# Kernel optimization log

Hardware: AMD Instinct MI355X
Metric: run time of the kernel (lower is better)

## Reference

```python
import jax, jax.numpy as jnp
import numpy as np

NUM_HEADS = 8
DIM = 256
NUM_Q = 1


def setup_inputs() -> dict:
    key = jax.random.key(0)
    ks = jax.random.split(key, 10)
    B, H, W, C = 4, 56, 56, DIM
    mask_h = mask_w = 7
    WinNum = mask_h * mask_w
    x = jax.random.normal(ks[0], (B, H, W, C), dtype=jnp.float32)
    clstoken = jax.random.normal(ks[1], (B, NUM_Q, C), dtype=jnp.float32)
    mask = jax.random.bernoulli(ks[2], 0.3, (B, WinNum, WinNum))
    # ensure each window attends to itself (avoid fully-masked rows)
    eye = jnp.eye(WinNum, dtype=bool)[None]
    mask = jnp.logical_or(mask, eye)
    Wqkv = jax.random.normal(ks[3], (C, 3 * C), dtype=jnp.float32) * (C ** -0.5)
    bqkv = jnp.zeros((3 * C,), dtype=jnp.float32)
    Wo = jax.random.normal(ks[4], (C, C), dtype=jnp.float32) * (C ** -0.5)
    bo = jnp.zeros((C,), dtype=jnp.float32)
    lepe_k = jax.random.normal(ks[5], (3, 3, 1, C), dtype=jnp.float32) * 0.1  # depthwise HWIO
    lepe_b = jnp.zeros((C,), dtype=jnp.float32)
    return {"x": x, "clstoken": clstoken, "mask": mask, "mask_h": mask_h,
            "mask_w": mask_w, "Wqkv": Wqkv, "bqkv": bqkv, "Wo": Wo, "bo": bo,
            "lepe_k": lepe_k, "lepe_b": lepe_b}


def _forward(x, clstoken, mask, mask_h, mask_w, Wqkv, bqkv, Wo, bo, lepe_k, lepe_b):
    B, H, W, C = x.shape
    num_q = clstoken.shape[1]
    Nh = NUM_HEADS
    Hd = C // Nh
    Win_h, Win_w = H // mask_h, W // mask_w
    WinPix = Win_h * Win_w
    WinNum = mask_h * mask_w
    L_win = H * W
    scale = C ** -0.5

    qkv = x @ Wqkv + bqkv                       # [B,H,W,3C]
    q, k, v = jnp.split(qkv, 3, axis=-1)
    qkv_cls = clstoken @ Wqkv + bqkv            # [B,Q,3C]
    q_cls, k_cls, v_cls = jnp.split(qkv_cls, 3, axis=-1)

    # depthwise lepe conv on v (NHWC)
    lepe = jax.lax.conv_general_dilated(
        v, lepe_k, window_strides=(1, 1), padding='SAME',
        dimension_numbers=('NHWC', 'HWIO', 'NHWC'), feature_group_count=C) + lepe_b

    def to_win(t):  # b (j h)(i w)(Nh Hd) -> b Nh (j i h w) Hd
        t = t.reshape(B, mask_h, Win_h, mask_w, Win_w, Nh, Hd)
        t = t.transpose(0, 5, 1, 3, 2, 4, 6)
        return t.reshape(B, Nh, L_win, Hd)

    def cls_heads(t):  # b q (Nh Hd) -> b Nh q Hd
        return t.reshape(B, num_q, Nh, Hd).transpose(0, 2, 1, 3)

    q_all = jnp.concatenate([to_win(q), cls_heads(q_cls)], axis=2)
    k_all = jnp.concatenate([to_win(k), cls_heads(k_cls)], axis=2)
    v_all = jnp.concatenate([to_win(v), cls_heads(v_cls)], axis=2)

    # token-level block mask; cls block (id WinNum) is globally visible
    blk = jnp.concatenate([jnp.arange(L_win) // WinPix,
                           jnp.full((num_q,), WinNum)])
    mask_ext = jnp.pad(mask, ((0, 0), (0, 1), (0, 1)), constant_values=True)
    tok_mask = mask_ext[:, blk[:, None], blk[None, :]]  # [B,L,L]

    scores = jnp.einsum('bnqd,bnkd->bnqk', q_all, k_all) * scale
    neg = jnp.finfo(scores.dtype).min
    scores = jnp.where(tok_mask[:, None], scores, neg)
    attn = jax.nn.softmax(scores, axis=-1)
    out = jnp.einsum('bnqk,bnkd->bnqd', attn, v_all)   # [B,Nh,L,Hd]

    cls_out = out[:, :, -num_q:, :]
    x_out = out[:, :, :-num_q, :]
    # b Nh (j i h w) Hd -> b (j h)(i w)(Nh Hd)
    x_out = x_out.reshape(B, Nh, mask_h, mask_w, Win_h, Win_w, Hd)
    x_out = x_out.transpose(0, 2, 4, 3, 5, 1, 6).reshape(B, H, W, C)
    cls_out = cls_out.transpose(0, 2, 1, 3).reshape(B, num_q, C)

    x_out = (x_out + lepe) @ Wo + bo
    cls_out = cls_out @ Wo + bo
    return x_out, cls_out


def reference(x, clstoken, mask, mask_h, mask_w, Wqkv, bqkv, Wo, bo, lepe_k, lepe_b):
    return _forward(x, clstoken, mask, mask_h, mask_w, Wqkv, bqkv, Wo, bo, lepe_k, lepe_b)
```

## Files before the change

kernel.cpp:

```cpp
#include <hip/hip_runtime.h>
#include <math.h>

#define B_      4
#define NH      8
#define HD      32
#define WINNUM  49
#define LWIN    3136
#define NTOK    3137
#define NPIX    12544
#define MROWS   12548
#define SCALE_L2E 0.09016844005556021f

typedef _Float16 half_t;
using half8  = __attribute__((ext_vector_type(8))) half_t;
using half4  = __attribute__((ext_vector_type(4))) half_t;
using f32x4  = __attribute__((ext_vector_type(4))) float;
using f32x16 = __attribute__((ext_vector_type(16))) float;

__device__ __forceinline__ unsigned pack2(float a, float b) {
    auto h = __builtin_amdgcn_cvt_pkrtz(a, b);
    return __builtin_bit_cast(unsigned, h);
}
__device__ __forceinline__ half8 as_h8(int4 v) {
    return __builtin_bit_cast(half8, v);
}

__global__ __launch_bounds__(256)
void prep(const float* __restrict__ x, const float* __restrict__ cls,
          const float* __restrict__ Wqkv, const float* __restrict__ Wo,
          half_t* __restrict__ xh, half_t* __restrict__ Wqkvt, half_t* __restrict__ Wot)
{
    const int idx = blockIdx.x * 256 + threadIdx.x;
    const int stride = gridDim.x * 256;
    for (int i = idx; i < MROWS * 256; i += stride) {
        int row = i >> 8, c = i & 255;
        float v = (row < NPIX) ? x[i] : cls[(row - NPIX) * 256 + c];
        xh[i] = (half_t)v;
    }
    for (int i = idx; i < 768 * 256; i += stride) {
        int n = i >> 8, k = i & 255;
        Wqkvt[i] = (half_t)Wqkv[k * 768 + n];
    }
    for (int i = idx; i < 256 * 256; i += stride) {
        int n = i >> 8, k = i & 255;
        Wot[i] = (half_t)Wo[k * 256 + n];
    }
}

__global__ __launch_bounds__(256)
void qkv_gemm(const half_t* __restrict__ xh, const half_t* __restrict__ Bt,
              const float* __restrict__ bqkv,
              half_t* __restrict__ qh, half_t* __restrict__ kh,
              half_t* __restrict__ khcls, half_t* __restrict__ vh,
              half_t* __restrict__ vplain)
{
    __shared__ __align__(16) short As[2][128 * 40];
    __shared__ __align__(16) short Bs[2][128 * 40];
    const int m0 = blockIdx.y * 128, n0 = blockIdx.x * 128;
    const int tid = threadIdx.x;
    const int lane = tid & 63, wv = tid >> 6;
    const int wm = wv >> 1, wn = wv & 1;
    const int qi = lane & 15, g = lane >> 4;
    f32x4 acc[4][4] = {};

    int4 ra[2], rb[2];
    auto issue = [&](int k0) {
#pragma unroll
        for (int i = 0; i < 2; ++i) {
            int ch = tid + 256 * i;
            int row = ch >> 2, kc = (ch & 3) * 8;
            int m = m0 + row;
            ra[i] = (m < MROWS) ? *(const int4*)(xh + (size_t)m * 256 + k0 + kc)
                                : make_int4(0, 0, 0, 0);
            rb[i] = *(const int4*)(Bt + (size_t)(n0 + row) * 256 + k0 + kc);
        }
    };
    auto commit = [&](int bu) {
#pragma unroll
        for (int i = 0; i < 2; ++i) {
            int ch = tid + 256 * i;
            int row = ch >> 2, kc = (ch & 3) * 8;
            *(int4*)&As[bu][row * 40 + kc] = ra[i];
            *(int4*)&Bs[bu][row * 40 + kc] = rb[i];
        }
    };

    issue(0); commit(0);
    __syncthreads();
    int buf = 0;
    for (int s = 0; s < 8; ++s) {
        if (s < 7) issue((s + 1) * 32);
        half8 af[4], bf[4];
#pragma unroll
        for (int f = 0; f < 4; ++f) {
            af[f] = *(const half8*)&As[buf][(wm * 64 + f * 16 + qi) * 40 + g * 8];
            bf[f] = *(const half8*)&Bs[buf][(wn * 64 + f * 16 + qi) * 40 + g * 8];
        }
#pragma unroll
        for (int fm = 0; fm < 4; ++fm)
#pragma unroll
            for (int fn = 0; fn < 4; ++fn)
                acc[fm][fn] = __builtin_amdgcn_mfma_f32_16x16x32_f16(af[fm], bf[fn], acc[fm][fn], 0, 0, 0);
        if (s < 7) commit(buf ^ 1);
        __syncthreads();
        buf ^= 1;
    }

    const int part = n0 >> 8;
    int nhv[4], dv[4];
    float bq[4];
#pragma unroll
    for (int fn = 0; fn < 4; ++fn) {
        int n = n0 + wn * 64 + fn * 16 + qi;
        bq[fn] = bqkv[n];
        int c = n & 255;
        nhv[fn] = c >> 5; dv[fn] = c & 31;
    }
#pragma unroll
    for (int fm = 0; fm < 4; ++fm) {
#pragma unroll
        for (int r = 0; r < 4; ++r) {
            int m = m0 + wm * 64 + fm * 16 + g * 4 + r;
            if (m >= MROWS) continue;
            int b, tok;
            if (m < NPIX) {
                b = m / LWIN;
                int p = m - b * LWIN;
                int hh = p / 56, ww = p - hh * 56;
                tok = ((hh >> 3) * 7 + (ww >> 3)) * 64 + ((hh & 7) << 3) + (ww & 7);
            } else { b = m - NPIX; tok = LWIN; }
#pragma unroll
            for (int fn = 0; fn < 4; ++fn) {
                float val = acc[fm][fn][r] + bq[fn];
                size_t bh = (size_t)(b * NH + nhv[fn]);
                int d = dv[fn];
                if (part == 0) {
                    qh[(bh * NTOK + tok) * 32 + d] = (half_t)(val * SCALE_L2E);
                } else if (part == 1) {
                    if (tok < LWIN) kh[(bh * WINNUM + (tok >> 6)) * 2560 + (tok & 63) * 40 + d] = (half_t)val;
                    else            khcls[bh * 32 + d] = (half_t)val;
                } else {
                    vplain[(bh * NTOK + tok) * 32 + d] = (half_t)val;
                    if (tok < LWIN) vh[(bh * WINNUM + (tok >> 6)) * 2560 + d * 80 + (tok & 63)] = (half_t)val;
                }
            }
        }
    }
}

__global__ __launch_bounds__(128)
void win_attn(const half_t* __restrict__ qh, const half_t* __restrict__ kh,
              const half_t* __restrict__ khcls, const half_t* __restrict__ vh,
              const half_t* __restrict__ vplain, const int* __restrict__ mask,
              half_t* __restrict__ tg, float* __restrict__ clspart)
{
    const int id = blockIdx.x;
    const int tid = threadIdx.x;
    __shared__ __align__(16) short Plds[2][32 * 72];
    __shared__ float redc[2 * 33];
    const int lane = tid & 63, wv = tid >> 6;

    if (id >= 1568) {
        const int cid = id - 1568;
        const int bh = cid >> 3;
        const int chunk = cid & 7;
        const int wstart = chunk * 6;
        const int nw = (chunk < 7) ? 6 : 7;
        const int nkeys = nw * 64;

        float q[32];
        {
            const half_t* qp = qh + ((size_t)bh * NTOK + LWIN) * 32;
#pragma unroll
            for (int d = 0; d < 32; ++d) q[d] = (float)qp[d];
        }
        float l = 0.f, o[32];
#pragma unroll
        for (int d = 0; d < 32; ++d) o[d] = 0.f;

        const half_t* kwb = kh + (size_t)bh * (WINNUM * 2560) + wstart * 2560;
        const half_t* vb  = vplain + ((size_t)bh * NTOK + wstart * 64) * 32;

        for (int kk = tid; kk < nkeys; kk += 128) {
            const half_t* kp = kwb + (kk >> 6) * 2560 + (kk & 63) * 40;
            float s = 0.f;
#pragma unroll
            for (int c8 = 0; c8 < 4; ++c8) {
                half8 kv = *(const half8*)(kp + c8 * 8);
#pragma unroll
                for (int j = 0; j < 8; ++j) s += q[c8 * 8 + j] * (float)kv[j];
            }
            float pp = exp2f(s);
            l += pp;
            const half_t* vp = vb + (size_t)kk * 32;
#pragma unroll
            for (int c8 = 0; c8 < 4; ++c8) {
                half8 vvv = *(const half8*)(vp + c8 * 8);
#pragma unroll
                for (int j = 0; j < 8; ++j) o[c8 * 8 + j] += pp * (float)vvv[j];
            }
        }
        if (chunk == 7 && tid == 0) {
            const half_t* kp = khcls + bh * 32;
            float s = 0.f;
#pragma unroll
            for (int d = 0; d < 32; ++d) s += q[d] * (float)kp[d];
            float pp = exp2f(s);
            l += pp;
            const half_t* vp = vplain + ((size_t)bh * NTOK + LWIN) * 32;
#pragma unroll
            for (int d = 0; d < 32; ++d) o[d] += pp * (float)vp[d];
        }
#pragma unroll
        for (int off = 1; off < 64; off <<= 1) {
            l += __shfl_xor(l, off);
#pragma unroll
            for (int d = 0; d < 32; ++d) o[d] += __shfl_xor(o[d], off);
        }
        if (lane == 0) {
#pragma unroll
            for (int d = 0; d < 32; ++d) redc[wv * 33 + d] = o[d];
            redc[wv * 33 + 32] = l;
        }
        __syncthreads();
        if (tid < 33) {
            clspart[(bh * 8 + chunk) * 33 + tid] = redc[tid] + redc[33 + tid];
        }
        return;
    }

    const int sw = (id & 7) * 196 + (id >> 3);
    const int wi = sw % 49;
    const int bh = sw / 49;
    const int b = bh >> 3, nh = bh & 7;

    const int qc = lane & 31;
    const int hb = lane >> 5;
    const int qbase = wi * 64 + wv * 32;

    const half_t* qp = qh + ((size_t)bh * NTOK + qbase + qc) * 32 + hb * 8;
    half8 aq0 = as_h8(*(const int4*)(qp));
    half8 aq1 = as_h8(*(const int4*)(qp + 16));

    half8 onesA = {};
    if (qc == 0) {
#pragma unroll
        for (int j = 0; j < 8; ++j) onesA[j] = (half_t)1.0f;
    }

    const f32x16 Z16 = {0.f,0.f,0.f,0.f,0.f,0.f,0.f,0.f,0.f,0.f,0.f,0.f,0.f,0.f,0.f,0.f};
    f32x16 acc   = Z16;
    f32x16 acc_l = Z16;

    const int* mrow = mask + (b * WINNUM + wi) * WINNUM;
    int mv = (lane < WINNUM) ? mrow[lane] : 0;
    unsigned long long rem = __ballot(mv != 0);

    const half_t* kwin = kh + (size_t)bh * (WINNUM * 2560);
    const half_t* vwin = vh + (size_t)bh * (WINNUM * 2560);

    short* pw = &Plds[wv][qc * 72];
    const short* prd = &Plds[wv][qc * 72 + hb * 8];

    while (rem) {
        const int wj = __builtin_ctzll(rem);
        rem &= rem - 1;
        const half_t* kb = kwin + wj * 2560 + qc * 40 + hb * 8;
        const half_t* vb = vwin + wj * 2560 + qc * 80 + hb * 8;
        int4 kf00 = *(const int4*)(kb);
        int4 kf01 = *(const int4*)(kb + 16);
        int4 kf10 = *(const int4*)(kb + 1280);
        int4 kf11 = *(const int4*)(kb + 1296);
        int4 vf0 = *(const int4*)(vb);
        int4 vf1 = *(const int4*)(vb + 16);
        int4 vf2 = *(const int4*)(vb + 32);
        int4 vf3 = *(const int4*)(vb + 48);

        f32x16 st[2];
        __builtin_amdgcn_s_setprio(1);
        st[0] = __builtin_amdgcn_mfma_f32_32x32x16_f16(as_h8(kf00), aq0, Z16, 0, 0, 0);
        st[1] = __builtin_amdgcn_mfma_f32_32x32x16_f16(as_h8(kf10), aq0, Z16, 0, 0, 0);
        st[0] = __builtin_amdgcn_mfma_f32_32x32x16_f16(as_h8(kf01), aq1, st[0], 0, 0, 0);
        st[1] = __builtin_amdgcn_mfma_f32_32x32x16_f16(as_h8(kf11), aq1, st[1], 0, 0, 0);
        __builtin_amdgcn_s_setprio(0);

#pragma unroll
        for (int t = 0; t < 2; ++t)
#pragma unroll
            for (int rb = 0; rb < 4; ++rb) {
                float p0 = exp2f(st[t][4 * rb + 0]);
                float p1 = exp2f(st[t][4 * rb + 1]);
                float p2 = exp2f(st[t][4 * rb + 2]);
                float p3 = exp2f(st[t][4 * rb + 3]);
                *(uint2*)&pw[t * 32 + 8 * rb + 4 * hb] =
                    make_uint2(pack2(p0, p1), pack2(p2, p3));
            }

        half8 pB0 = *(const half8*)(prd);
        half8 pB1 = *(const half8*)(prd + 16);
        half8 pB2 = *(const half8*)(prd + 32);
        half8 pB3 = *(const half8*)(prd + 48);
        __builtin_amdgcn_s_setprio(1);
        acc   = __builtin_amdgcn_mfma_f32_32x32x16_f16(as_h8(vf0), pB0, acc, 0, 0, 0);
        acc_l = __builtin_amdgcn_mfma_f32_32x32x16_f16(onesA, pB0, acc_l, 0, 0, 0);
        acc   = __builtin_amdgcn_mfma_f32_32x32x16_f16(as_h8(vf1), pB1, acc, 0, 0, 0);
        acc_l = __builtin_amdgcn_mfma_f32_32x32x16_f16(onesA, pB1, acc_l, 0, 0, 0);
        acc   = __builtin_amdgcn_mfma_f32_32x32x16_f16(as_h8(vf2), pB2, acc, 0, 0, 0);
        acc_l = __builtin_amdgcn_mfma_f32_32x32x16_f16(onesA, pB2, acc_l, 0, 0, 0);
        acc   = __builtin_amdgcn_mfma_f32_32x32x16_f16(as_h8(vf3), pB3, acc, 0, 0, 0);
        acc_l = __builtin_amdgcn_mfma_f32_32x32x16_f16(onesA, pB3, acc_l, 0, 0, 0);
        __builtin_amdgcn_s_setprio(0);
    }

    float lwin = __shfl(acc_l[0], qc);

    float sc = 0.f;
    {
        const half_t* kcb = khcls + bh * 32 + hb * 8;
        half8 kc0 = *(const half8*)(kcb);
        half8 kc1 = *(const half8*)(kcb + 16);
#pragma unroll
        for (int j = 0; j < 8; ++j)
            sc += (float)aq0[j] * (float)kc0[j] + (float)aq1[j] * (float)kc1[j];
        sc += __shfl_xor(sc, 32);
    }
    float pc = exp2f(sc);
    float l = lwin + pc;
    {
        const half_t* vcb = vplain + ((size_t)bh * NTOK + LWIN) * 32;
#pragma unroll
        for (int rb = 0; rb < 4; ++rb) {
            half4 vc = *(const half4*)(vcb + 8 * rb + 4 * hb);
#pragma unroll
            for (int r = 0; r < 4; ++r) acc[4 * rb + r] += pc * (float)vc[r];
        }
    }

    {
        float inv = 1.f / l;
        int kk = wv * 32 + qc;
        int hh = (wi / 7) * 8 + (kk >> 3);
        int ww = (wi % 7) * 8 + (kk & 7);
        size_t pix = (size_t)b * LWIN + hh * 56 + ww;
        half_t* tp = tg + pix * 256 + nh * 32;
#pragma unroll
        for (int rb = 0; rb < 4; ++rb) {
            half4 hv;
#pragma unroll
            for (int r = 0; r < 4; ++r) hv[r] = (half_t)(acc[4 * rb + r] * inv);
            *(half4*)(tp + 8 * rb + 4 * hb) = hv;
        }
    }
}

__global__ __launch_bounds__(256)
void lepe_add(const half_t* __restrict__ vplain, const float* __restrict__ lk,
              const float* __restrict__ lb, const float* __restrict__ clspart,
              half_t* __restrict__ tg)
{
    if (blockIdx.x == 1568) {
        const int c = threadIdx.x;
        const int nh = c >> 5, d = c & 31;
#pragma unroll
        for (int b = 0; b < 4; ++b) {
            int bh = b * NH + nh;
            float os = 0.f, ls = 0.f;
#pragma unroll
            for (int ch = 0; ch < 8; ++ch) {
                os += clspart[(bh * 8 + ch) * 33 + d];
                ls += clspart[(bh * 8 + ch) * 33 + 32];
            }
            tg[(size_t)(NPIX + b) * 256 + c] = (half_t)(os / ls);
        }
        return;
    }
    const int gidx = blockIdx.x * 256 + threadIdx.x;
    const int pix = gidx >> 5, cg = gidx & 31;
    const int c0 = cg * 8;
    const int b = pix / LWIN, p = pix - b * LWIN;
    const int hh = p / 56, ww = p - hh * 56;
    const int nh = c0 >> 5, d0 = c0 & 31;
    const half_t* vb = vplain + (size_t)(b * NH + nh) * NTOK * 32 + d0;

    float s[8];
#pragma unroll
    for (int j = 0; j < 8; ++j) s[j] = lb[c0 + j];
#pragma unroll
    for (int dh = -1; dh <= 1; ++dh) {
        int hn = hh + dh;
        if (hn < 0 || hn >= 56) continue;
#pragma unroll
        for (int dw = -1; dw <= 1; ++dw) {
            int wn = ww + dw;
            if (wn < 0 || wn >= 56) continue;
            int tok = ((hn >> 3) * 7 + (wn >> 3)) * 64 + ((hn & 7) << 3) + (wn & 7);
            half8 vvv = *(const half8*)(vb + (size_t)tok * 32);
            const float* kk = lk + ((dh + 1) * 3 + (dw + 1)) * 256 + c0;
#pragma unroll
            for (int j = 0; j < 8; ++j) s[j] += (float)vvv[j] * kk[j];
        }
    }
    half_t* tp = tg + (size_t)pix * 256 + c0;
    half8 cur = *(const half8*)tp;
    half8 outv;
#pragma unroll
    for (int j = 0; j < 8; ++j) outv[j] = (half_t)((float)cur[j] + s[j]);
    *(half8*)tp = outv;
}

__global__ __launch_bounds__(256)
void out_gemm(const half_t* __restrict__ th, const half_t* __restrict__ Bt,
              const float* __restrict__ bo, float* __restrict__ out)
{
    __shared__ __align__(16) short As[2][64 * 40];
    __shared__ __align__(16) short Bs[2][128 * 40];
    const int m0 = blockIdx.y * 64, n0 = blockIdx.x * 128;
    const int tid = threadIdx.x;
    const int lane = tid & 63, wv = tid >> 6;
    const int wm = wv >> 1, wn = wv & 1;
    const int qi = lane & 15, g = lane >> 4;
    f32x4 acc[2][4] = {};

    int4 ra, rb[2];
    auto issue = [&](int k0) {
        {
            int row = tid >> 2, kc = (tid & 3) * 8;
            int m = m0 + row;
            ra = (m < MROWS) ? *(const int4*)(th + (size_t)m * 256 + k0 + kc)
                             : make_int4(0, 0, 0, 0);
        }
#pragma unroll
        for (int i = 0; i < 2; ++i) {
            int ch = tid + 256 * i;
            int row = ch >> 2, kc = (ch & 3) * 8;
            rb[i] = *(const int4*)(Bt + (size_t)(n0 + row) * 256 + k0 + kc);
        }
    };
    auto commit = [&](int bu) {
        {
            int row = tid >> 2, kc = (tid & 3) * 8;
            *(int4*)&As[bu][row * 40 + kc] = ra;
        }
#pragma unroll
        for (int i = 0; i < 2; ++i) {
            int ch = tid + 256 * i;
            int row = ch >> 2, kc = (ch & 3) * 8;
            *(int4*)&Bs[bu][row * 40 + kc] = rb[i];
        }
    };

    issue(0); commit(0);
    __syncthreads();
    int buf = 0;
    for (int s = 0; s < 8; ++s) {
        if (s < 7) issue((s + 1) * 32);
        half8 af[2], bf[4];
#pragma unroll
        for (int f = 0; f < 2; ++f)
            af[f] = *(const half8*)&As[buf][(wm * 32 + f * 16 + qi) * 40 + g * 8];
#pragma unroll
        for (int f = 0; f < 4; ++f)
            bf[f] = *(const half8*)&Bs[buf][(wn * 64 + f * 16 + qi) * 40 + g * 8];
#pragma unroll
        for (int fm = 0; fm < 2; ++fm)
#pragma unroll
            for (int fn = 0; fn < 4; ++fn)
                acc[fm][fn] = __builtin_amdgcn_mfma_f32_16x16x32_f16(af[fm], bf[fn], acc[fm][fn], 0, 0, 0);
        if (s < 7) commit(buf ^ 1);
        __syncthreads();
        buf ^= 1;
    }

    float bov[4];
    int nn[4];
#pragma unroll
    for (int fn = 0; fn < 4; ++fn) {
        nn[fn] = n0 + wn * 64 + fn * 16 + qi;
        bov[fn] = bo[nn[fn]];
    }
#pragma unroll
    for (int fm = 0; fm < 2; ++fm)
#pragma unroll
        for (int r = 0; r < 4; ++r) {
            int m = m0 + wm * 32 + fm * 16 + g * 4 + r;
            if (m >= MROWS) continue;
#pragma unroll
            for (int fn = 0; fn < 4; ++fn)
                out[(size_t)m * 256 + nn[fn]] = acc[fm][fn][r] + bov[fn];
        }
}

extern "C" void kernel_launch(void* const* d_in, const int* in_sizes, int n_in,
                              void* d_out, int out_size, void* d_ws, size_t ws_size,
                              hipStream_t stream)
{
    const float* x    = (const float*)d_in[0];
    const float* cls  = (const float*)d_in[1];
    const int*   mask = (const int*)d_in[2];
    const float* Wqkv = (const float*)d_in[5];
    const float* bqkv = (const float*)d_in[6];
    const float* Wo   = (const float*)d_in[7];
    const float* bo   = (const float*)d_in[8];
    const float* lk   = (const float*)d_in[9];
    const float* lb   = (const float*)d_in[10];
    float* out = (float*)d_out;

    char* w = (char*)d_ws;
    half_t* xh     = (half_t*)w;  w += 6424576;
    half_t* qh     = (half_t*)w;  w += 6424576;
    half_t* kh     = (half_t*)w;  w += 8028160;
    half_t* khcls  = (half_t*)w;  w += 2048;
    half_t* vh     = (half_t*)w;  w += 8028160;
    half_t* vplain = (half_t*)w;  w += 6424576;
    half_t* Wqkvt  = (half_t*)w;  w += 393216;
    half_t* Wot    = (half_t*)w;  w += 131072;
    half_t* th     = (half_t*)w;  w += 6424576;
    float*  clspart= (float*)w;   w += 33792;

    prep<<<1600, 256, 0, stream>>>(x, cls, Wqkv, Wo, xh, Wqkvt, Wot);
    qkv_gemm<<<dim3(6, 99), 256, 0, stream>>>(xh, Wqkvt, bqkv, qh, kh, khcls, vh, vplain);
    win_attn<<<1824, 128, 0, stream>>>(qh, kh, khcls, vh, vplain, mask, th, clspart);
    lepe_add<<<1569, 256, 0, stream>>>(vplain, lk, lb, clspart, th);
    out_gemm<<<dim3(2, 197), 256, 0, stream>>>(th, Wot, bo, out);
}
```

Measured before the change: 125.2 us.

## Split window-attention key windows across wave pairs with double-buffered loads

Blocks for window attention grow from 128 to 256 threads. Each pair of waves now processes alternating visible key windows for the same 32 queries, and the two partial accumulators are combined through shared memory before normalization and the cls-token contribution. The main loop also double-buffers the K/V register loads so the next window's fetch is issued while the current one is computed. This aims to hide global-load latency and add parallelism per query tile, at the cost of more registers, an extra LDS reduction with two barriers, and a serial mask-splitting loop.

```diff
diff --git a/kernel.cpp b/kernel.cpp
--- a/kernel.cpp
+++ b/kernel.cpp
@@ -148,7 +148,7 @@
     }
 }
 
-__global__ __launch_bounds__(128)
+__global__ __launch_bounds__(256)
 void win_attn(const half_t* __restrict__ qh, const half_t* __restrict__ kh,
               const half_t* __restrict__ khcls, const half_t* __restrict__ vh,
               const half_t* __restrict__ vplain, const int* __restrict__ mask,
@@ -156,8 +156,8 @@
 {
     const int id = blockIdx.x;
     const int tid = threadIdx.x;
-    __shared__ __align__(16) short Plds[2][32 * 72];
-    __shared__ float redc[2 * 33];
+    __shared__ __align__(16) short Plds[4][32 * 72];
+    __shared__ float redc[4 * 33];
     const int lane = tid & 63, wv = tid >> 6;
 
     if (id >= 1568) {
@@ -181,7 +181,7 @@
         const half_t* kwb = kh + (size_t)bh * (WINNUM * 2560) + wstart * 2560;
         const half_t* vb  = vplain + ((size_t)bh * NTOK + wstart * 64) * 32;
 
-        for (int kk = tid; kk < nkeys; kk += 128) {
+        for (int kk = tid; kk < nkeys; kk += 256) {
             const half_t* kp = kwb + (kk >> 6) * 2560 + (kk & 63) * 40;
             float s = 0.f;
 #pragma unroll
@@ -224,7 +224,8 @@
         }
         __syncthreads();
         if (tid < 33) {
-            clspart[(bh * 8 + chunk) * 33 + tid] = redc[tid] + redc[33 + tid];
+            clspart[(bh * 8 + chunk) * 33 + tid] =
+                redc[tid] + redc[33 + tid] + redc[66 + tid] + redc[99 + tid];
         }
         return;
     }
@@ -234,9 +235,11 @@
     const int bh = sw / 49;
     const int b = bh >> 3, nh = bh & 7;
 
+    const int qhalf = wv & 1;
+    const int par   = wv >> 1;
     const int qc = lane & 31;
     const int hb = lane >> 5;
-    const int qbase = wi * 64 + wv * 32;
+    const int qbase = wi * 64 + qhalf * 32;
 
     const half_t* qp = qh + ((size_t)bh * NTOK + qbase + qc) * 32 + hb * 8;
     half8 aq0 = as_h8(*(const int4*)(qp));
@@ -254,48 +257,52 @@
 
     const int* mrow = mask + (b * WINNUM + wi) * WINNUM;
     int mv = (lane < WINNUM) ? mrow[lane] : 0;
-    unsigned long long rem = __ballot(mv != 0);
+    unsigned long long all = __ballot(mv != 0);
+    unsigned long long rem = 0;
+    {
+        unsigned long long t = all;
+        int i = 0;
+        while (t) {
+            int j = __builtin_ctzll(t);
+            t &= t - 1;
+            if ((i & 1) == par) rem |= (1ull << j);
+            ++i;
+        }
+    }
 
     const half_t* kwin = kh + (size_t)bh * (WINNUM * 2560);
     const half_t* vwin = vh + (size_t)bh * (WINNUM * 2560);
+    const int koff = qc * 40 + hb * 8;
+    const int voff = qc * 80 + hb * 8;
 
     short* pw = &Plds[wv][qc * 72];
     const short* prd = &Plds[wv][qc * 72 + hb * 8];
 
-    while (rem) {
-        const int wj = __builtin_ctzll(rem);
-        rem &= rem - 1;
-        const half_t* kb = kwin + wj * 2560 + qc * 40 + hb * 8;
-        const half_t* vb = vwin + wj * 2560 + qc * 80 + hb * 8;
-        int4 kf00 = *(const int4*)(kb);
-        int4 kf01 = *(const int4*)(kb + 16);
-        int4 kf10 = *(const int4*)(kb + 1280);
-        int4 kf11 = *(const int4*)(kb + 1296);
-        int4 vf0 = *(const int4*)(vb);
-        int4 vf1 = *(const int4*)(vb + 16);
-        int4 vf2 = *(const int4*)(vb + 32);
-        int4 vf3 = *(const int4*)(vb + 48);
-
-        f32x16 st[2];
+    auto COMPUTE = [&](int4 kf00, int4 kf01, int4 kf10, int4 kf11,
+                       int4 vf0, int4 vf1, int4 vf2, int4 vf3) {
+        f32x16 st0, st1;
         __builtin_amdgcn_s_setprio(1);
-        st[0] = __builtin_amdgcn_mfma_f32_32x32x16_f16(as_h8(kf00), aq0, Z16, 0, 0, 0);
-        st[1] = __builtin_amdgcn_mfma_f32_32x32x16_f16(as_h8(kf10), aq0, Z16, 0, 0, 0);
-        st[0] = __builtin_amdgcn_mfma_f32_32x32x16_f16(as_h8(kf01), aq1, st[0], 0, 0, 0);
-        st[1] = __builtin_amdgcn_mfma_f32_32x32x16_f16(as_h8(kf11), aq1, st[1], 0, 0, 0);
+        st0 = __builtin_amdgcn_mfma_f32_32x32x16_f16(as_h8(kf00), aq0, Z16, 0, 0, 0);
+        st1 = __builtin_amdgcn_mfma_f32_32x32x16_f16(as_h8(kf10), aq0, Z16, 0, 0, 0);
+        st0 = __builtin_amdgcn_mfma_f32_32x32x16_f16(as_h8(kf01), aq1, st0, 0, 0, 0);
+        st1 = __builtin_amdgcn_mfma_f32_32x32x16_f16(as_h8(kf11), aq1, st1, 0, 0, 0);
         __builtin_amdgcn_s_setprio(0);
-
-#pragma unroll
-        for (int t = 0; t < 2; ++t)
-#pragma unroll
-            for (int rb = 0; rb < 4; ++rb) {
-                float p0 = exp2f(st[t][4 * rb + 0]);
-                float p1 = exp2f(st[t][4 * rb + 1]);
-                float p2 = exp2f(st[t][4 * rb + 2]);
-                float p3 = exp2f(st[t][4 * rb + 3]);
-                *(uint2*)&pw[t * 32 + 8 * rb + 4 * hb] =
-                    make_uint2(pack2(p0, p1), pack2(p2, p3));
-            }
-
+#pragma unroll
+        for (int rb = 0; rb < 4; ++rb) {
+            float p0 = exp2f(st0[4 * rb + 0]);
+            float p1 = exp2f(st0[4 * rb + 1]);
+            float p2 = exp2f(st0[4 * rb + 2]);
+            float p3 = exp2f(st0[4 * rb + 3]);
+            *(uint2*)&pw[8 * rb + 4 * hb] = make_uint2(pack2(p0, p1), pack2(p2, p3));
+        }
+#pragma unroll
+        for (int rb = 0; rb < 4; ++rb) {
+            float p0 = exp2f(st1[4 * rb + 0]);
+            float p1 = exp2f(st1[4 * rb + 1]);
+            float p2 = exp2f(st1[4 * rb + 2]);
+            float p3 = exp2f(st1[4 * rb + 3]);
+            *(uint2*)&pw[32 + 8 * rb + 4 * hb] = make_uint2(pack2(p0, p1), pack2(p2, p3));
+        }
         half8 pB0 = *(const half8*)(prd);
         half8 pB1 = *(const half8*)(prd + 16);
         half8 pB2 = *(const half8*)(prd + 32);
@@ -310,35 +317,88 @@
         acc   = __builtin_amdgcn_mfma_f32_32x32x16_f16(as_h8(vf3), pB3, acc, 0, 0, 0);
         acc_l = __builtin_amdgcn_mfma_f32_32x32x16_f16(onesA, pB3, acc_l, 0, 0, 0);
         __builtin_amdgcn_s_setprio(0);
-    }
-
-    float lwin = __shfl(acc_l[0], qc);
-
-    float sc = 0.f;
-    {
-        const half_t* kcb = khcls + bh * 32 + hb * 8;
-        half8 kc0 = *(const half8*)(kcb);
-        half8 kc1 = *(const half8*)(kcb + 16);
-#pragma unroll
-        for (int j = 0; j < 8; ++j)
-            sc += (float)aq0[j] * (float)kc0[j] + (float)aq1[j] * (float)kc1[j];
-        sc += __shfl_xor(sc, 32);
-    }
-    float pc = exp2f(sc);
-    float l = lwin + pc;
-    {
-        const half_t* vcb = vplain + ((size_t)bh * NTOK + LWIN) * 32;
-#pragma unroll
-        for (int rb = 0; rb < 4; ++rb) {
-            half4 vc = *(const half4*)(vcb + 8 * rb + 4 * hb);
-#pragma unroll
-            for (int r = 0; r < 4; ++r) acc[4 * rb + r] += pc * (float)vc[r];
-        }
-    }
-
-    {
+    };
+
+    int4 a0, a1, a2, a3, a4, a5, a6, a7;
+    int4 b0, b1, b2, b3, b4, b5, b6, b7;
+    auto ISSUE_A = [&](int wj) {
+        const half_t* kb = kwin + wj * 2560 + koff;
+        const half_t* vb = vwin + wj * 2560 + voff;
+        a0 = *(const int4*)(kb);        a1 = *(const int4*)(kb + 16);
+        a2 = *(const int4*)(kb + 1280); a3 = *(const int4*)(kb + 1296);
+        a4 = *(const int4*)(vb);        a5 = *(const int4*)(vb + 16);
+        a6 = *(const int4*)(vb + 32);   a7 = *(const int4*)(vb + 48);
+    };
+    auto ISSUE_B = [&](int wj) {
+        const half_t* kb = kwin + wj * 2560 + koff;
+        const half_t* vb = vwin + wj * 2560 + voff;
+        b0 = *(const int4*)(kb);        b1 = *(const int4*)(kb + 16);
+        b2 = *(const int4*)(kb + 1280); b3 = *(const int4*)(kb + 1296);
+        b4 = *(const int4*)(vb);        b5 = *(const int4*)(vb + 16);
+        b6 = *(const int4*)(vb + 32);   b7 = *(const int4*)(vb + 48);
+    };
+
+    bool haveA = false;
+    if (rem) {
+        int wj = __builtin_ctzll(rem); rem &= rem - 1;
+        ISSUE_A(wj); haveA = true;
+    }
+    while (haveA) {
+        bool haveB = false;
+        if (rem) {
+            int wj = __builtin_ctzll(rem); rem &= rem - 1;
+            ISSUE_B(wj); haveB = true;
+        }
+        COMPUTE(a0, a1, a2, a3, a4, a5, a6, a7);
+        if (!haveB) break;
+        haveA = false;
+        if (rem) {
+            int wj = __builtin_ctzll(rem); rem &= rem - 1;
+            ISSUE_A(wj); haveA = true;
+        }
+        COMPUTE(b0, b1, b2, b3, b4, b5, b6, b7);
+    }
+
+    __syncthreads();
+    float* mb = (float*)Plds;
+    if (par == 1) {
+        float* dst = mb + qhalf * 1088;
+#pragma unroll
+        for (int r = 0; r < 16; ++r) dst[r * 64 + lane] = acc[r];
+        dst[1024 + lane] = acc_l[0];
+    }
+    __syncthreads();
+    if (par == 0) {
+        const float* src = mb + qhalf * 1088;
+#pragma unroll
+        for (int r = 0; r < 16; ++r) acc[r] += src[r * 64 + lane];
+        float accl0 = acc_l[0] + src[1024 + lane];
+        float lwin = __shfl(accl0, qc);
+
+        float sc = 0.f;
+        {
+            const half_t* kcb = khcls + bh * 32 + hb * 8;
+            half8 kc0 = *(const half8*)(kcb);
+            half8 kc1 = *(const half8*)(kcb + 16);
+#pragma unroll
+            for (int j = 0; j < 8; ++j)
+                sc += (float)aq0[j] * (float)kc0[j] + (float)aq1[j] * (float)kc1[j];
+            sc += __shfl_xor(sc, 32);
+        }
+        float pc = exp2f(sc);
+        float l = lwin + pc;
+        {
+            const half_t* vcb = vplain + ((size_t)bh * NTOK + LWIN) * 32;
+#pragma unroll
+            for (int rb = 0; rb < 4; ++rb) {
+                half4 vc = *(const half4*)(vcb + 8 * rb + 4 * hb);
+#pragma unroll
+                for (int r = 0; r < 4; ++r) acc[4 * rb + r] += pc * (float)vc[r];
+            }
+        }
+
         float inv = 1.f / l;
-        int kk = wv * 32 + qc;
+        int kk = qhalf * 32 + qc;
         int hh = (wi / 7) * 8 + (kk >> 3);
         int ww = (wi % 7) * 8 + (kk & 7);
         size_t pix = (size_t)b * LWIN + hh * 56 + ww;
@@ -519,7 +579,7 @@
 
     prep<<<1600, 256, 0, stream>>>(x, cls, Wqkv, Wo, xh, Wqkvt, Wot);
     qkv_gemm<<<dim3(6, 99), 256, 0, stream>>>(xh, Wqkvt, bqkv, qh, kh, khcls, vh, vplain);
-    win_attn<<<1824, 128, 0, stream>>>(qh, kh, khcls, vh, vplain, mask, th, clspart);
+    win_attn<<<1824, 256, 0, stream>>>(qh, kh, khcls, vh, vplain, mask, th, clspart);
     lepe_add<<<1569, 256, 0, stream>>>(vplain, lk, lb, clspart, th);
     out_gemm<<<dim3(2, 197), 256, 0, stream>>>(th, Wot, bo, out);
 }
```

After: 124.6 us. No clear change (-0.5%).
